# Optimization experiments

Measured on AMD Instinct MI355X. Metric: run time of the kernel, lower is better.

The kernel has to match this reference:

```python
import jax, jax.numpy as jnp
import numpy as np

# Problem sizes (match init_kwargs / input_specs)
B, NV, NE, SUBSTEPS = 4, 100000, 400000, 10
DT = 0.01          # integration timestep (init arg dt)
K_SPRING = 1000.0  # spring stiffness
MASS = 1.0         # per-particle mass
DAMP = 0.999       # velocity damping
ACT_SCALE = 0.1
EPS = 1e-6         # avoid div-by-zero on degenerate springs
GRAVITY = jnp.array([0.0, -9.8, 0.0], dtype=jnp.float32)


def setup_inputs() -> dict:
    key = jax.random.key(0)
    k1, k2, k3, k4, k5 = jax.random.split(key, 5)
    input_action = jax.random.normal(k1, (B, NE), dtype=jnp.float32)
    input_pos = jax.random.normal(k2, (B, NV, 3), dtype=jnp.float32)
    input_vel = 0.1 * jax.random.normal(k3, (B, NV, 3), dtype=jnp.float32)
    rest_len = jax.random.uniform(k4, (NE,), dtype=jnp.float32)
    edges = jax.random.randint(k5, (NE, 2), 0, NV, dtype=jnp.int32)
    return {"input_action": input_action, "input_pos": input_pos,
            "input_vel": input_vel, "rest_len": rest_len, "edges": edges}


def reference(input_action, input_pos, input_vel, rest_len, edges):
    """Mass-spring substep integrator over a spring-particle graph.

    Returns (output_pos, output_vel), each [B, SUBSTEPS+1, NV, 3]:
    the trajectory including the initial state, matching the torch buffers.
    """
    i_idx, j_idx = edges[:, 0], edges[:, 1]
    # Actuation changes the effective rest length per spring: [B, NE]
    rest_eff = rest_len[None, :] * (1.0 + ACT_SCALE * jnp.tanh(input_action))

    def step(carry, _):
        pos, vel = carry                      # [B, NV, 3]
        d = pos[:, j_idx] - pos[:, i_idx]     # gather endpoints: [B, NE, 3]
        length = jnp.sqrt(jnp.sum(d * d, axis=-1) + EPS)   # [B, NE]
        # Hookean force on node i pulling toward node j
        f = (K_SPRING * (length - rest_eff) / length)[..., None] * d  # [B, NE, 3]
        # Scatter-add spring forces to particles (Newton's third law)
        f_node = jnp.zeros_like(pos).at[:, i_idx].add(f).at[:, j_idx].add(-f)
        vel_n = (vel + DT * (f_node / MASS + GRAVITY)) * DAMP
        pos_n = pos + DT * vel_n              # symplectic Euler
        return (pos_n, vel_n), (pos_n, vel_n)

    _, (p_traj, v_traj) = jax.lax.scan(step, (input_pos, input_vel), None,
                                       length=SUBSTEPS)
    # [S, B, NV, 3] -> [B, S, NV, 3]; prepend initial state -> [B, S+1, NV, 3]
    out_pos = jnp.concatenate([input_pos[:, None], jnp.moveaxis(p_traj, 0, 1)], axis=1)
    out_vel = jnp.concatenate([input_vel[:, None], jnp.moveaxis(v_traj, 0, 1)], axis=1)
    return out_pos, out_vel
```

## Files before the change

### kernel.cpp

```cpp
#include <hip/hip_runtime.h>

#define NV 100000
#define NE 400000
#define BB 4
#define NSUB 10
constexpr float DT        = 0.01f;
constexpr float K_SPRING  = 1000.0f;
constexpr float DAMP      = 0.999f;
constexpr float ACT_SCALE = 0.1f;
constexpr float EPS       = 1e-6f;

#define VEL_BASE ((size_t)BB * (NSUB + 1) * NV * 3)
#define NBLK ((NV + 255) / 256)
#define PADCAP (2 * NE + 3 * NV + 64)

typedef float fv4 __attribute__((ext_vector_type(4)));
typedef int   iv4 __attribute__((ext_vector_type(4)));


__global__ void init_all(const float* __restrict__ pos0,
                         const float* __restrict__ vel0,
                         float* __restrict__ out,
                         float4* __restrict__ posT,
                         float4* __restrict__ velT) {
    int gid = blockIdx.x * blockDim.x + threadIdx.x;
    if (gid >= BB * NV) return;
    int b = gid & 3, v = gid >> 2;
    const float* ps = pos0 + ((size_t)b * NV + v) * 3;
    const float* vs = vel0 + ((size_t)b * NV + v) * 3;
    float px = ps[0], py = ps[1], pz = ps[2];
    float vx = vs[0], vy = vs[1], vz = vs[2];
    posT[gid] = make_float4(px, py, pz, 0.f);
    if (velT) velT[gid] = make_float4(vx, vy, vz, 0.f);
    size_t o = ((size_t)(b * (NSUB + 1)) * NV + v) * 3;
    out[o + 0] = px; out[o + 1] = py; out[o + 2] = pz;
    out[VEL_BASE + o + 0] = vx; out[VEL_BASE + o + 1] = vy; out[VEL_BASE + o + 2] = vz;
}

__global__ void zero_deg(int* __restrict__ deg) {
    int v = blockIdx.x * blockDim.x + threadIdx.x;
    if (v < NV) deg[v] = 0;
}

__global__ void count_kernel(const int2* __restrict__ edges, int* __restrict__ deg) {
    int e = blockIdx.x * blockDim.x + threadIdx.x;
    if (e >= NE) return;
    int2 ed = edges[e];
    atomicAdd(&deg[ed.x], 1);
    atomicAdd(&deg[ed.y], 1);
}

__device__ __forceinline__ int padded(int d) { return (d + 3) & ~3; }

__global__ void scan_partials(const int* __restrict__ deg, int* __restrict__ bsum) {
    __shared__ int red[256];
    int i = blockIdx.x * 256 + threadIdx.x;
    red[threadIdx.x] = (i < NV) ? padded(deg[i]) : 0;
    __syncthreads();
    for (int off = 128; off > 0; off >>= 1) {
        if (threadIdx.x < off) red[threadIdx.x] += red[threadIdx.x + off];
        __syncthreads();
    }
    if (threadIdx.x == 0) bsum[blockIdx.x] = red[0];
}

__global__ void scan_bsums(int* __restrict__ bsum) {
    __shared__ int s[512];
    int t = threadIdx.x;
    s[t] = (t < NBLK) ? bsum[t] : 0;
    __syncthreads();
    for (int off = 1; off < 512; off <<= 1) {
        int v = (t >= off) ? s[t - off] : 0;
        __syncthreads();
        s[t] += v;
        __syncthreads();
    }
    if (t < NBLK) bsum[t] = (t == 0) ? 0 : s[t - 1];
}

__global__ void scan_write(const int* __restrict__ deg, const int* __restrict__ bsum,
                           int* __restrict__ offs, int* __restrict__ cursor,
                           int* __restrict__ lo, float* __restrict__ lre2) {
    __shared__ int s[256];
    int i = blockIdx.x * 256 + threadIdx.x;
    int draw = (i < NV) ? deg[i] : 0;
    int d = padded(draw);
    s[threadIdx.x] = d;
    __syncthreads();
    for (int off = 1; off < 256; off <<= 1) {
        int v = (threadIdx.x >= off) ? s[threadIdx.x - off] : 0;
        __syncthreads();
        s[threadIdx.x] += v;
        __syncthreads();
    }
    if (i <= NV - 1) {
        int excl = bsum[blockIdx.x] + s[threadIdx.x] - d;
        offs[i] = excl; cursor[i] = excl;
        if (i == NV - 1) offs[NV] = excl + d;
        for (int k = excl + draw; k < excl + d; ++k) {
            lo[k] = i;
            size_t kb = (size_t)(k & ~3) * 4 + (k & 3);
            #pragma unroll
            for (int b = 0; b < BB; ++b) lre2[kb + 4 * b] = 0.f;
        }
    }
}

__global__ void fill_fat(const int2* __restrict__ edges,
                         const float* __restrict__ action,
                         const float* __restrict__ rest_len,
                         int* __restrict__ cursor,
                         int* __restrict__ lo,
                         float* __restrict__ lre2) {
    int e = blockIdx.x * blockDim.x + threadIdx.x;
    if (e >= NE) return;
    int2 ed = edges[e];
    float krl = K_SPRING * rest_len[e];
    fv4 re;
    #pragma unroll
    for (int b = 0; b < BB; ++b)
        re[b] = krl * (1.0f + ACT_SCALE * tanhf(action[b * NE + e]));
    int p = atomicAdd(&cursor[ed.x], 1);
    int q = atomicAdd(&cursor[ed.y], 1);
    lo[p] = ed.y; lo[q] = ed.x;
    size_t pb = (size_t)(p & ~3) * 4 + (p & 3);
    size_t qb = (size_t)(q & ~3) * 4 + (q & 3);
    #pragma unroll
    for (int b = 0; b < BB; ++b) {
        lre2[pb + 4 * b] = re[b];
        lre2[qb + 4 * b] = re[b];
    }
}

template <bool VELT>
__global__ void substep_ks(float* __restrict__ out,
                           const float4* __restrict__ posT,
                           float4* __restrict__ posTn,
                           float4* __restrict__ velT,
                           const int* __restrict__ lo,
                           const float* __restrict__ lre2,
                           const int* __restrict__ offs, int s) {
    int gid = blockIdx.x * blockDim.x + threadIdx.x;
    if (gid >= 2 * BB * NV) return;
    int b = gid & 3, h = (gid >> 2) & 1, v = gid >> 3;

    float4 p = posT[v * 4 + b];
    float fx = 0.f, fy = 0.f, fz = 0.f;

    int start = offs[v], end = offs[v + 1];
    int nc0 = ((((end - start) >> 2) + 1) >> 1) << 2;
    int k    = h ? (start + nc0) : start;
    int kend = h ? end : (start + nc0);

#define ACC(q, kre) do { \
        float dx = (q).x - p.x, dy = (q).y - p.y, dz = (q).z - p.z; \
        float d2 = fmaf(dx, dx, fmaf(dy, dy, fmaf(dz, dz, EPS))); \
        float rs = rsqrtf(d2); \
        float t  = fmaf(-(kre), rs, K_SPRING); \
        fx = fmaf(t, dx, fx); fy = fmaf(t, dy, fy); fz = fmaf(t, dz, fz); } while (0)

    for (; k + 7 < kend; k += 8) {
        iv4 oA = __builtin_nontemporal_load((const iv4*)(lo + k));
        iv4 oB = __builtin_nontemporal_load((const iv4*)(lo + k + 4));
        fv4 rA = __builtin_nontemporal_load((const fv4*)(lre2 + 4 * (size_t)k + 4 * b));
        fv4 rB = __builtin_nontemporal_load((const fv4*)(lre2 + 4 * (size_t)(k + 4) + 4 * b));
        float4 qA0 = posT[oA.x * 4 + b];
        float4 qA1 = posT[oA.y * 4 + b];
        float4 qA2 = posT[oA.z * 4 + b];
        float4 qA3 = posT[oA.w * 4 + b];
        float4 qB0 = posT[oB.x * 4 + b];
        float4 qB1 = posT[oB.y * 4 + b];
        float4 qB2 = posT[oB.z * 4 + b];
        float4 qB3 = posT[oB.w * 4 + b];
        ACC(qA0, rA[0]); ACC(qA1, rA[1]); ACC(qA2, rA[2]); ACC(qA3, rA[3]);
        ACC(qB0, rB[0]); ACC(qB1, rB[1]); ACC(qB2, rB[2]); ACC(qB3, rB[3]);
    }
    if (k < kend) {
        iv4 o = __builtin_nontemporal_load((const iv4*)(lo + k));
        fv4 r = __builtin_nontemporal_load((const fv4*)(lre2 + 4 * (size_t)k + 4 * b));
        float4 q0 = posT[o.x * 4 + b];
        float4 q1 = posT[o.y * 4 + b];
        float4 q2 = posT[o.z * 4 + b];
        float4 q3 = posT[o.w * 4 + b];
        ACC(q0, r[0]); ACC(q1, r[1]); ACC(q2, r[2]); ACC(q3, r[3]);
    }
#undef ACC

    fx += __shfl_xor(fx, 4);
    fy += __shfl_xor(fy, 4);
    fz += __shfl_xor(fz, 4);

    if (h == 0) {
        int tg = v * 4 + b;
        size_t cur = ((size_t)(b * (NSUB + 1) + s)) * NV * 3 + (size_t)v * 3;
        size_t nxt = cur + (size_t)NV * 3;

        float vcx, vcy, vcz;
        if (VELT) {
            float4 vc = velT[tg];
            vcx = vc.x; vcy = vc.y; vcz = vc.z;
        } else {
            vcx = out[VEL_BASE + cur + 0];
            vcy = out[VEL_BASE + cur + 1];
            vcz = out[VEL_BASE + cur + 2];
        }
        float vx = (vcx + DT * fx) * DAMP;
        float vy = (vcy + DT * (fy - 9.8f)) * DAMP;
        float vz = (vcz + DT * fz) * DAMP;
        float pxn = p.x + DT * vx, pyn = p.y + DT * vy, pzn = p.z + DT * vz;

        __builtin_nontemporal_store(pxn, out + nxt + 0);
        __builtin_nontemporal_store(pyn, out + nxt + 1);
        __builtin_nontemporal_store(pzn, out + nxt + 2);
        if (VELT) {
            __builtin_nontemporal_store(vx, out + VEL_BASE + nxt + 0);
            __builtin_nontemporal_store(vy, out + VEL_BASE + nxt + 1);
            __builtin_nontemporal_store(vz, out + VEL_BASE + nxt + 2);
            velT[tg] = make_float4(vx, vy, vz, 0.f);
        } else {
            out[VEL_BASE + nxt + 0] = vx;
            out[VEL_BASE + nxt + 1] = vy;
            out[VEL_BASE + nxt + 2] = vz;
        }
        posTn[tg] = make_float4(pxn, pyn, pzn, 0.f);
    }
}

extern "C" void kernel_launch(void* const* d_in, const int* in_sizes, int n_in,
                              void* d_out, int out_size, void* d_ws, size_t ws_size,
                              hipStream_t stream) {
    const float* action   = (const float*)d_in[0];
    const float* pos0     = (const float*)d_in[1];
    const float* vel0     = (const float*)d_in[2];
    const float* rest_len = (const float*)d_in[3];
    const int2*  edges    = (const int2*)d_in[4];
    float* out = (float*)d_out;

    char* ws = (char*)d_ws;
    size_t off = 0;
    int* deg    = (int*)(ws + off); off += (size_t)NV * 4;
    int* offs   = (int*)(ws + off); off += (size_t)(NV + 1) * 4;
    int* cursor = (int*)(ws + off); off += (size_t)NV * 4;
    int* bsum   = (int*)(ws + off); off += (size_t)(NBLK + 4) * 4;
    off = (off + 63) & ~(size_t)63;
    float4* pTa = (float4*)(ws + off); off += (size_t)NV * BB * 16;
    float4* pTb = (float4*)(ws + off); off += (size_t)NV * BB * 16;
    int*   lo   = (int*)(ws + off);   off += (size_t)PADCAP * 4;
    float* lre2 = (float*)(ws + off); off += (size_t)PADCAP * 16;
    float4* vT = (float4*)(ws + off);
    const bool velt = ws_size >= off + (size_t)NV * BB * 16;

    const int nBV  = BB * NV;
    const int nKS  = 2 * BB * NV;

    init_all<<<(nBV + 255) / 256, 256, 0, stream>>>(pos0, vel0, out, pTa, velt ? vT : nullptr);
    zero_deg<<<NBLK, 256, 0, stream>>>(deg);
    count_kernel<<<(NE + 255) / 256, 256, 0, stream>>>(edges, deg);
    scan_partials<<<NBLK, 256, 0, stream>>>(deg, bsum);
    scan_bsums<<<1, 512, 0, stream>>>(bsum);
    scan_write<<<NBLK, 256, 0, stream>>>(deg, bsum, offs, cursor, lo, lre2);
    fill_fat<<<(NE + 255) / 256, 256, 0, stream>>>(edges, action, rest_len, cursor, lo, lre2);

    for (int s = 0; s < NSUB; ++s) {
        float4* pc = (s & 1) ? pTb : pTa;
        float4* pn = (s & 1) ? pTa : pTb;
        if (velt) {
            substep_ks<true><<<(nKS + 255) / 256, 256, 0, stream>>>(
                out, pc, pn, vT, lo, lre2, offs, s);
        } else {
            substep_ks<false><<<(nKS + 255) / 256, 256, 0, stream>>>(
                out, pc, pn, nullptr, lo, lre2, offs, s);
        }
    }
}
```

Baseline: 348.7 us.

## Split CSR fill into compact slot scatter plus coalesced expansion pass

Computes per-edge effective rest lengths in the degree-counting kernel. The adjacency fill then scatters only compact (neighbor, edge) pairs to atomically allocated slots, and a separate linear pass expands them into the neighbor and rest-length arrays. The aim is to replace wide random scattered writes of four rest lengths per slot with narrow 8-byte scattered writes followed by coalesced writes. The cost is an extra kernel launch, extra workspace and a second read of the slot array, and the path only runs when the workspace is large enough.

```diff
diff --git a/kernel.cpp b/kernel.cpp
--- a/kernel.cpp
+++ b/kernel.cpp
@@ -16,6 +16,7 @@
 
 typedef float fv4 __attribute__((ext_vector_type(4)));
 typedef int   iv4 __attribute__((ext_vector_type(4)));
+typedef int   iv2 __attribute__((ext_vector_type(2)));
 
 
 __global__ void init_all(const float* __restrict__ pos0,
@@ -42,12 +43,24 @@
     if (v < NV) deg[v] = 0;
 }
 
-__global__ void count_kernel(const int2* __restrict__ edges, int* __restrict__ deg) {
+__global__ void count_rt(const int2* __restrict__ edges,
+                         const float* __restrict__ action,
+                         const float* __restrict__ rest_len,
+                         int* __restrict__ deg,
+                         fv4* __restrict__ rT) {
     int e = blockIdx.x * blockDim.x + threadIdx.x;
     if (e >= NE) return;
     int2 ed = edges[e];
     atomicAdd(&deg[ed.x], 1);
     atomicAdd(&deg[ed.y], 1);
+    if (rT) {
+        float krl = K_SPRING * rest_len[e];
+        fv4 re;
+        #pragma unroll
+        for (int b = 0; b < BB; ++b)
+            re[b] = krl * (1.0f + ACT_SCALE * tanhf(action[b * NE + e]));
+        rT[e] = re;
+    }
 }
 
 __device__ __forceinline__ int padded(int d) { return (d + 3) & ~3; }
@@ -80,6 +93,7 @@
 
 __global__ void scan_write(const int* __restrict__ deg, const int* __restrict__ bsum,
                            int* __restrict__ offs, int* __restrict__ cursor,
+                           iv2* __restrict__ islot,
                            int* __restrict__ lo, float* __restrict__ lre2) {
     __shared__ int s[256];
     int i = blockIdx.x * 256 + threadIdx.x;
@@ -98,12 +112,46 @@
         offs[i] = excl; cursor[i] = excl;
         if (i == NV - 1) offs[NV] = excl + d;
         for (int k = excl + draw; k < excl + d; ++k) {
-            lo[k] = i;
-            size_t kb = (size_t)(k & ~3) * 4 + (k & 3);
-            #pragma unroll
-            for (int b = 0; b < BB; ++b) lre2[kb + 4 * b] = 0.f;
+            if (islot) {
+                iv2 t; t.x = i; t.y = -1;
+                islot[k] = t;
+            } else {
+                lo[k] = i;
+                size_t kb = (size_t)(k & ~3) * 4 + (k & 3);
+                #pragma unroll
+                for (int b = 0; b < BB; ++b) lre2[kb + 4 * b] = 0.f;
+            }
         }
     }
+}
+
+__global__ void scatter_k(const int2* __restrict__ edges,
+                          int* __restrict__ cursor,
+                          iv2* __restrict__ islot) {
+    int e = blockIdx.x * blockDim.x + threadIdx.x;
+    if (e >= NE) return;
+    int2 ed = edges[e];
+    int p = atomicAdd(&cursor[ed.x], 1);
+    int q = atomicAdd(&cursor[ed.y], 1);
+    iv2 a; a.x = ed.y; a.y = e;
+    iv2 c; c.x = ed.x; c.y = e;
+    islot[p] = a;
+    islot[q] = c;
+}
+
+__global__ void expand_k(const iv2* __restrict__ islot,
+                         const fv4* __restrict__ rT,
+                         const int* __restrict__ offs,
+                         int* __restrict__ lo,
+                         float* __restrict__ lre2) {
+    int k = blockIdx.x * blockDim.x + threadIdx.x;
+    if (k >= offs[NV]) return;
+    iv2 t = islot[k];
+    lo[k] = t.x;
+    fv4 r = (t.y >= 0) ? rT[t.y] : (fv4)(0.f);
+    size_t kb = (size_t)(k & ~3) * 4 + (k & 3);
+    #pragma unroll
+    for (int b = 0; b < BB; ++b) lre2[kb + 4 * b] = r[b];
 }
 
 __global__ void fill_fat(const int2* __restrict__ edges,
@@ -249,17 +297,28 @@
     float* lre2 = (float*)(ws + off); off += (size_t)PADCAP * 16;
     float4* vT = (float4*)(ws + off);
     const bool velt = ws_size >= off + (size_t)NV * BB * 16;
+    size_t off2 = off + (size_t)NV * BB * 16;
+    fv4* rT    = (fv4*)(ws + off2); off2 += (size_t)NE * 16;
+    iv2* islot = (iv2*)(ws + off2); off2 += (size_t)PADCAP * 8;
+    const bool twophase = velt && (ws_size >= off2);
 
     const int nBV  = BB * NV;
     const int nKS  = 2 * BB * NV;
 
     init_all<<<(nBV + 255) / 256, 256, 0, stream>>>(pos0, vel0, out, pTa, velt ? vT : nullptr);
     zero_deg<<<NBLK, 256, 0, stream>>>(deg);
-    count_kernel<<<(NE + 255) / 256, 256, 0, stream>>>(edges, deg);
+    count_rt<<<(NE + 255) / 256, 256, 0, stream>>>(edges, action, rest_len, deg,
+                                                   twophase ? rT : nullptr);
     scan_partials<<<NBLK, 256, 0, stream>>>(deg, bsum);
     scan_bsums<<<1, 512, 0, stream>>>(bsum);
-    scan_write<<<NBLK, 256, 0, stream>>>(deg, bsum, offs, cursor, lo, lre2);
-    fill_fat<<<(NE + 255) / 256, 256, 0, stream>>>(edges, action, rest_len, cursor, lo, lre2);
+    scan_write<<<NBLK, 256, 0, stream>>>(deg, bsum, offs, cursor,
+                                         twophase ? islot : nullptr, lo, lre2);
+    if (twophase) {
+        scatter_k<<<(NE + 255) / 256, 256, 0, stream>>>(edges, cursor, islot);
+        expand_k<<<(PADCAP + 255) / 256, 256, 0, stream>>>(islot, rT, offs, lo, lre2);
+    } else {
+        fill_fat<<<(NE + 255) / 256, 256, 0, stream>>>(edges, action, rest_len, cursor, lo, lre2);
+    }
 
     for (int s = 0; s < NSUB; ++s) {
         float4* pc = (s & 1) ? pTb : pTa;
```

After: 353.7 us. No clear change (+1.4%).
